# Performance work log

Hardware: AMD Instinct MI355X
Metric: run time of the kernel (lower is better)

The kernel has to match this reference:

```python
import jax, jax.numpy as jnp
import numpy as np


def setup_inputs() -> dict:
    key = jax.random.key(0)
    k_q, k_k, k_v, k_xd, k_yd = jax.random.split(key, 5)
    B, L, H, E, K = 8, 4096, 2048, 512, 64
    return {
        "queries": jax.random.normal(k_q, (B, L, E), dtype=jnp.float32),
        "keys": jax.random.normal(k_k, (B, L, E), dtype=jnp.float32),
        "values": jax.random.normal(k_v, (B, L, E), dtype=jnp.float32),
        "x_date": jax.random.normal(k_xd, (B, L, K), dtype=jnp.float32),
        "y_date": jax.random.normal(k_yd, (B, H, K), dtype=jnp.float32),
    }


def reference(queries, keys, values, x_date, y_date):
    # queries/keys are unused in the original forward's math (only shapes).
    k = x_date.shape[-1]
    scale = 1.0 / float(np.sqrt(k))  # self.scale is None -> 1/sqrt(k)
    # scores: [B, L, H] from date features
    scores = jnp.einsum('blk,bhk->blh', x_date, y_date)
    # softmax over target axis H (dim=-1), numerically stable
    A = jax.nn.softmax(scale * scores, axis=-1)  # [B, L, H]
    # weighted reduction over source axis L -> [B, H, E]
    V = jnp.einsum('ble,blh->bhe', values, A)
    return V
```

## Files before the change

### kernel.cpp

```cpp
#include <hip/hip_runtime.h>
#include <hip/hip_bf16.h>

#define BN 8
#define LN 4096
#define HN 2048
#define EN 512
#define KN 64
#define LT 32
#define NIT 128

typedef __attribute__((ext_vector_type(8))) short bf16x8;
typedef __attribute__((ext_vector_type(4))) float f32x4;
typedef __attribute__((ext_vector_type(4))) unsigned u32x4;

__device__ __forceinline__ short f2b(float x) {
  union { float f; unsigned u; } v; v.f = x;
  unsigned r = v.u + 0x7fffu + ((v.u >> 16) & 1u);
  return (short)(r >> 16);
}

__device__ __forceinline__ bf16x8 cvt8s(const float* __restrict__ p, float s) {
  f32x4 a = *(const f32x4*)(p);
  f32x4 b = *(const f32x4*)(p + 4);
  bf16x8 r;
  r[0] = f2b(a[0] * s); r[1] = f2b(a[1] * s); r[2] = f2b(a[2] * s); r[3] = f2b(a[3] * s);
  r[4] = f2b(b[0] * s); r[5] = f2b(b[1] * s); r[6] = f2b(b[2] * s); r[7] = f2b(b[3] * s);
  return r;
}

__device__ __forceinline__ void gload16(const void* g, void* s) {
  __builtin_amdgcn_global_load_lds(
      (const __attribute__((address_space(1))) unsigned int*)(unsigned long long)g,
      (__attribute__((address_space(3))) unsigned int*)(unsigned int)(unsigned long long)s,
      16, 0, 0);
}

__global__ __launch_bounds__(256) void k_prep(const float* __restrict__ vals,
                                              short* __restrict__ valsT,
                                              const float* __restrict__ xd,
                                              short* __restrict__ xo,
                                              const float* __restrict__ yd,
                                              short* __restrict__ yo,
                                              float* __restrict__ ps) {
  __shared__ unsigned trT[2048];
  const int bx = blockIdx.x;
  const int tid = threadIdx.x;
  const float c0 = 0.125f * 1.4426950408889634f;
  if (bx < 1536) {
    const float* src;
    short* dst;
    float scale;
    int i;
    if (bx < 1024) { i = bx * 256 + tid; src = xd; dst = xo; scale = c0; }
    else           { i = (bx - 1024) * 256 + tid; src = yd; dst = yo; scale = 1.0f; }
    *(bf16x8*)(dst + (size_t)i * 8) = cvt8s(src + (size_t)i * 8, scale);
  } else if (bx < 5632) {
    const int idx = bx - 1536;
    const int b = idx >> 9;
    const int e0 = ((idx >> 6) & 7) * 64;
    const int l0 = (idx & 63) * 64;
    {
      int lr2 = tid >> 3;
      int ec = (tid & 7) * 8;
      const float* r0 = vals + ((size_t)b * LN + l0 + 2 * lr2) * EN + e0 + ec;
      const float* r1 = r0 + EN;
      f32x4 a0 = *(const f32x4*)r0, a1 = *(const f32x4*)(r0 + 4);
      f32x4 cc0 = *(const f32x4*)r1, cc1 = *(const f32x4*)(r1 + 4);
#pragma unroll
      for (int j = 0; j < 8; ++j) {
        float lo = (j < 4) ? a0[j] : a1[j - 4];
        float hi = (j < 4) ? cc0[j] : cc1[j - 4];
        unsigned dw = (unsigned)(unsigned short)f2b(lo) |
                      ((unsigned)(unsigned short)f2b(hi) << 16);
        int e = ec + j;
        int sz = (((e >> 3) ^ e) & 7) << 2;
        trT[e * 32 + (lr2 ^ sz)] = dw;
      }
    }
    __syncthreads();
    {
      int er = tid >> 2, lq = (tid & 3) * 8;
      int sr = ((er >> 3) ^ er) & 7;
      const unsigned* base = trT + er * 32;
      u32x4 u0 = *(const u32x4*)(base + ((((lq >> 2) + 0) ^ sr) << 2));
      u32x4 u1 = *(const u32x4*)(base + ((((lq >> 2) + 1) ^ sr) << 2));
      short* dst = valsT + ((size_t)b * EN + e0 + er) * LN + l0 + 2 * lq;
      *(u32x4*)dst = u0;
      *(u32x4*)(dst + 8) = u1;
    }
  } else {
    const int idx = bx - 5632;
    const int b = (idx >> 5) & 7, hc = idx >> 8;
    const int w = tid >> 6, lane = tid & 63;
    const int row = lane & 15, g = lane >> 4;
    const int lb = (idx & 31) * 128 + w * 32;
    const size_t bL = (size_t)b * LN, bH = (size_t)b * HN;
    bf16x8 xa[2][2];
#pragma unroll
    for (int lt = 0; lt < 2; ++lt) {
      const float* xp = xd + (bL + lb + lt * 16 + row) * KN + g * 8;
      xa[lt][0] = cvt8s(xp, c0);
      xa[lt][1] = cvt8s(xp + 32, c0);
    }
    float s[2][4] = {{0.f, 0.f, 0.f, 0.f}, {0.f, 0.f, 0.f, 0.f}};
    const float* ybase = yd + (bH + hc * 512 + row) * KN + g * 8;
#pragma unroll 2
    for (int it = 0; it < 32; ++it) {
      const float* yp = ybase + (size_t)it * (16 * KN);
      bf16x8 y0 = cvt8s(yp, 1.0f);
      bf16x8 y1 = cvt8s(yp + 32, 1.0f);
#pragma unroll
      for (int lt = 0; lt < 2; ++lt) {
        f32x4 a = {0.f, 0.f, 0.f, 0.f};
        a = __builtin_amdgcn_mfma_f32_16x16x32_bf16(xa[lt][0], y0, a, 0, 0, 0);
        a = __builtin_amdgcn_mfma_f32_16x16x32_bf16(xa[lt][1], y1, a, 0, 0, 0);
#pragma unroll
        for (int r = 0; r < 4; ++r) s[lt][r] += __builtin_amdgcn_exp2f(a[r]);
      }
    }
#pragma unroll
    for (int d = 1; d < 16; d <<= 1)
#pragma unroll
      for (int lt = 0; lt < 2; ++lt)
#pragma unroll
        for (int r = 0; r < 4; ++r) s[lt][r] += __shfl_xor(s[lt][r], d);
    if (row == 0) {
#pragma unroll
      for (int lt = 0; lt < 2; ++lt)
#pragma unroll
        for (int r = 0; r < 4; ++r)
          ps[(size_t)hc * (BN * LN) + bL + lb + lt * 16 + 4 * g + r] = s[lt][r];
    }
  }
}

__global__ void k_comb(const float* __restrict__ ps, float* __restrict__ wv) {
  int idx = blockIdx.x * 256 + threadIdx.x;
  float z = ps[idx] + ps[BN * LN + idx] + ps[2 * BN * LN + idx] + ps[3 * BN * LN + idx];
  wv[idx] = 1.0f / z;
}

__global__ __launch_bounds__(256, 2) void k_main7(
    const short* __restrict__ valsT, const short* __restrict__ xb,
    const short* __restrict__ yb, const float* __restrict__ wv,
    float* __restrict__ out) {
  __shared__ __align__(16) char smem[70016];
  const int tid = threadIdx.x;
  const int w = tid >> 6, lane = tid & 63;
  const int row = lane & 15, g = lane >> 4;

  const int f = blockIdx.x;
  const int b = f & 7;
  const int rest = f >> 3;
  const int hb = (rest & 31) * 64;
  const int eb = (rest >> 5) * 256;
  const size_t bL = (size_t)b * LN, bH = (size_t)b * HN;
  const int wbase = __builtin_amdgcn_readfirstlane(tid & ~63);

  const short* vsrc[4];
#pragma unroll
  for (int j = 0; j < 4; ++j) {
    int i = j * 256 + tid;
    int e = i >> 2, sl = (i & 3) ^ ((e >> 1) & 3);
    vsrc[j] = valsT + (((size_t)b * EN + eb + e) << 12) + 8 * sl;
  }
  const short* xsrc = xb + ((bL + (tid >> 3)) << 6) + 8 * ((tid & 7) ^ ((tid >> 3) & 7));
  const float* ssrc = wv + bL + 4 * tid;

  auto stage = [&](int t) {
    int m3 = t % 3;
    gload16(xsrc + ((size_t)t << 11), smem + 49152 + m3 * 4096 + wbase * 16);
    if (tid < 8)
      gload16(ssrc + t * 32, smem + 69632 + m3 * 128);
#pragma unroll
    for (int j = 0; j < 4; ++j)
      gload16(vsrc[j] + t * 32, smem + m3 * 16384 + j * 4096 + wbase * 16);
  };

  bf16x8 ya0, ya1;
  {
    const short* yp = yb + ((bH + hb + w * 16 + row) << 6) + 8 * g;
    ya0 = *(const bf16x8*)yp;
    ya1 = *(const bf16x8*)(yp + 32);
  }
  int xoffA[2], xoffB[2], poff[2], swoff[2];
#pragma unroll
  for (int lt = 0; lt < 2; ++lt) {
    int lr = lt * 16 + row;
    int sp0 = g ^ (lr & 7);
    xoffA[lt] = (lr << 7) + (sp0 << 4);
    xoffB[lt] = (lr << 7) + ((sp0 ^ 4) << 4);
    int hq1 = w * 16 + row;
    poff[lt] = hq1 * 64 + (((2 * lt + (g >> 1)) ^ ((hq1 >> 1) & 3)) << 4) + (g & 1) * 8;
    swoff[lt] = lt * 16 + 4 * g;
  }

  int paoff[4], vboff[4];
#pragma unroll
  for (int at = 0; at < 4; ++at) {
    int hq = at * 16 + row;
    paoff[at] = hq * 64 + ((g ^ ((hq >> 1) & 3)) << 4);
  }
#pragma unroll
  for (int n = 0; n < 4; ++n) {
    int el = w * 64 + n * 16 + row;
    vboff[n] = el * 64 + ((g ^ ((el >> 1) & 3)) << 4);
  }

  f32x4 acc[4][4];
#pragma unroll
  for (int at = 0; at < 4; ++at)
#pragma unroll
    for (int n = 0; n < 4; ++n) acc[at][n] = (f32x4){0.f, 0.f, 0.f, 0.f};

  auto produce = [&](int t) {
    const char* xbuf = smem + 49152 + (t % 3) * 4096;
    const float* swp = (const float*)(smem + 69632 + (t % 3) * 128);
    char* pdst = smem + 61440 + (t & 1) * 4096;
#pragma unroll
    for (int lt = 0; lt < 2; ++lt) {
      bf16x8 xa0 = *(const bf16x8*)(xbuf + xoffA[lt]);
      bf16x8 xa1 = *(const bf16x8*)(xbuf + xoffB[lt]);
      f32x4 sws = *(const f32x4*)(swp + swoff[lt]);
      f32x4 s4 = {0.f, 0.f, 0.f, 0.f};
      s4 = __builtin_amdgcn_mfma_f32_16x16x32_bf16(xa0, ya0, s4, 0, 0, 0);
      s4 = __builtin_amdgcn_mfma_f32_16x16x32_bf16(xa1, ya1, s4, 0, 0, 0);
      unsigned u0 = (unsigned)(unsigned short)f2b(__builtin_amdgcn_exp2f(s4[0]) * sws[0]) |
                    ((unsigned)(unsigned short)f2b(__builtin_amdgcn_exp2f(s4[1]) * sws[1]) << 16);
      unsigned u1 = (unsigned)(unsigned short)f2b(__builtin_amdgcn_exp2f(s4[2]) * sws[2]) |
                    ((unsigned)(unsigned short)f2b(__builtin_amdgcn_exp2f(s4[3]) * sws[3]) << 16);
      *(unsigned long long*)(pdst + poff[lt]) =
          (unsigned long long)u0 | ((unsigned long long)u1 << 32);
    }
  };

  auto consume = [&](int t) {
    const char* vbuf = smem + (t % 3) * 16384;
    const char* pbuf = smem + 61440 + (t & 1) * 4096;
    bf16x8 pa0 = *(const bf16x8*)(pbuf + paoff[0]);
    bf16x8 pa1 = *(const bf16x8*)(pbuf + paoff[1]);
    bf16x8 pa2 = *(const bf16x8*)(pbuf + paoff[2]);
    bf16x8 pa3 = *(const bf16x8*)(pbuf + paoff[3]);
    bf16x8 vb0 = *(const bf16x8*)(vbuf + vboff[0]);
    bf16x8 vb1 = *(const bf16x8*)(vbuf + vboff[1]);
    bf16x8 vb2 = *(const bf16x8*)(vbuf + vboff[2]);
    bf16x8 vb3 = *(const bf16x8*)(vbuf + vboff[3]);
    __builtin_amdgcn_s_setprio(1);
    acc[0][0] = __builtin_amdgcn_mfma_f32_16x16x32_bf16(pa0, vb0, acc[0][0], 0, 0, 0);
    acc[1][0] = __builtin_amdgcn_mfma_f32_16x16x32_bf16(pa1, vb0, acc[1][0], 0, 0, 0);
    acc[2][0] = __builtin_amdgcn_mfma_f32_16x16x32_bf16(pa2, vb0, acc[2][0], 0, 0, 0);
    acc[3][0] = __builtin_amdgcn_mfma_f32_16x16x32_bf16(pa3, vb0, acc[3][0], 0, 0, 0);
    acc[0][1] = __builtin_amdgcn_mfma_f32_16x16x32_bf16(pa0, vb1, acc[0][1], 0, 0, 0);
    acc[1][1] = __builtin_amdgcn_mfma_f32_16x16x32_bf16(pa1, vb1, acc[1][1], 0, 0, 0);
    acc[2][1] = __builtin_amdgcn_mfma_f32_16x16x32_bf16(pa2, vb1, acc[2][1], 0, 0, 0);
    acc[3][1] = __builtin_amdgcn_mfma_f32_16x16x32_bf16(pa3, vb1, acc[3][1], 0, 0, 0);
    acc[0][2] = __builtin_amdgcn_mfma_f32_16x16x32_bf16(pa0, vb2, acc[0][2], 0, 0, 0);
    acc[1][2] = __builtin_amdgcn_mfma_f32_16x16x32_bf16(pa1, vb2, acc[1][2], 0, 0, 0);
    acc[2][2] = __builtin_amdgcn_mfma_f32_16x16x32_bf16(pa2, vb2, acc[2][2], 0, 0, 0);
    acc[3][2] = __builtin_amdgcn_mfma_f32_16x16x32_bf16(pa3, vb2, acc[3][2], 0, 0, 0);
    acc[0][3] = __builtin_amdgcn_mfma_f32_16x16x32_bf16(pa0, vb3, acc[0][3], 0, 0, 0);
    acc[1][3] = __builtin_amdgcn_mfma_f32_16x16x32_bf16(pa1, vb3, acc[1][3], 0, 0, 0);
    acc[2][3] = __builtin_amdgcn_mfma_f32_16x16x32_bf16(pa2, vb3, acc[2][3], 0, 0, 0);
    acc[3][3] = __builtin_amdgcn_mfma_f32_16x16x32_bf16(pa3, vb3, acc[3][3], 0, 0, 0);
    __builtin_amdgcn_s_setprio(0);
  };

  stage(0);
  stage(1);
  asm volatile("s_waitcnt vmcnt(4)" ::: "memory");
  __builtin_amdgcn_s_barrier();
  asm volatile("" ::: "memory");
  produce(0);
  asm volatile("s_waitcnt lgkmcnt(0)" ::: "memory");
  __builtin_amdgcn_s_barrier();
  asm volatile("" ::: "memory");

  for (int it = 0; it < NIT; ++it) {
    if (it + 2 < NIT) stage(it + 2);
    if (it + 1 < NIT) produce(it + 1);
    consume(it);
    if (it + 1 < NIT) {
      if (it + 2 < NIT)
        asm volatile("s_waitcnt vmcnt(4) lgkmcnt(0)" ::: "memory");
      else
        asm volatile("s_waitcnt vmcnt(0) lgkmcnt(0)" ::: "memory");
      __builtin_amdgcn_s_barrier();
      asm volatile("" ::: "memory");
    }
  }

#pragma unroll
  for (int at = 0; at < 4; ++at)
#pragma unroll
    for (int n = 0; n < 4; ++n)
#pragma unroll
      for (int r = 0; r < 4; ++r) {
        int h = hb + at * 16 + 4 * g + r;
        int e = eb + w * 64 + n * 16 + row;
        out[(bH + h) * (size_t)EN + e] = acc[at][n][r];
      }
}

__global__ __launch_bounds__(256) void k_stats_o(const float* __restrict__ xd,
                                                 const float* __restrict__ yd,
                                                 float* __restrict__ mz) {
  const int b = blockIdx.y;
  const int w = threadIdx.x >> 6;
  const int lane = threadIdx.x & 63;
  const int row = lane & 15, g = lane >> 4;
  const int lb = blockIdx.x * 64 + w * 16;
  const float* xp = xd + ((size_t)b * LN + lb + row) * KN + g * 8;
  bf16x8 a0 = cvt8s(xp, 1.0f), a1 = cvt8s(xp + 32, 1.0f);
  float m[4], s[4];
#pragma unroll
  for (int r = 0; r < 4; ++r) { m[r] = -1e30f; s[r] = 0.f; }
  const float* ybp = yd + ((size_t)b * HN + row) * KN + g * 8;
  for (int h0 = 0; h0 < HN; h0 += 16) {
    bf16x8 b0 = cvt8s(ybp + (size_t)h0 * KN, 1.0f);
    bf16x8 b1 = cvt8s(ybp + (size_t)h0 * KN + 32, 1.0f);
    f32x4 acc = {0.f, 0.f, 0.f, 0.f};
    acc = __builtin_amdgcn_mfma_f32_16x16x32_bf16(a0, b0, acc, 0, 0, 0);
    acc = __builtin_amdgcn_mfma_f32_16x16x32_bf16(a1, b1, acc, 0, 0, 0);
#pragma unroll
    for (int r = 0; r < 4; ++r) {
      float v = acc[r] * 0.125f;
      float mn = fmaxf(m[r], v);
      s[r] = s[r] * __expf(m[r] - mn) + __expf(v - mn);
      m[r] = mn;
    }
  }
#pragma unroll
  for (int d = 1; d < 16; d <<= 1) {
#pragma unroll
    for (int r = 0; r < 4; ++r) {
      float mo = __shfl_xor(m[r], d);
      float so = __shfl_xor(s[r], d);
      float mn = fmaxf(m[r], mo);
      s[r] = s[r] * __expf(m[r] - mn) + so * __expf(mo - mn);
      m[r] = mn;
    }
  }
  if (row == 0) {
#pragma unroll
    for (int r = 0; r < 4; ++r) {
      size_t idx = (size_t)b * LN + lb + 4 * g + r;
      mz[idx] = m[r];
      mz[(size_t)BN * LN + idx] = 1.0f / s[r];
    }
  }
}

__global__ __launch_bounds__(512) void k_main_o(const float* __restrict__ vals,
                                                const float* __restrict__ xd,
                                                const float* __restrict__ yd,
                                                const float* __restrict__ mz,
                                                float* __restrict__ out) {
  __shared__ short vT[256][34];
  __shared__ short pT[128][34];
  __shared__ short xT[32][72];
  __shared__ float smm[32], smz[32];
  const int b = blockIdx.z;
  const int hb = blockIdx.x * 128;
  const int eb = blockIdx.y * 256;
  const int tid = threadIdx.x;
  const int w = tid >> 6, lane = tid & 63;
  const int row = lane & 15, g = lane >> 4;
  const float* yp = yd + ((size_t)b * HN + hb + w * 16 + row) * KN + g * 8;
  bf16x8 ya0 = cvt8s(yp, 1.0f), ya1 = cvt8s(yp + 32, 1.0f);
  f32x4 acc[16];
#pragma unroll
  for (int n = 0; n < 16; ++n) acc[n] = (f32x4){0.f, 0.f, 0.f, 0.f};
  const float* mzb = mz + (size_t)b * LN;
  const float* rzb = mz + (size_t)BN * LN + (size_t)b * LN;
  for (int l0 = 0; l0 < LN; l0 += 32) {
    __syncthreads();
    {
      int xl = tid >> 4, xk = (tid & 15) * 4;
      f32x4 xv = *(const f32x4*)(xd + ((size_t)b * LN + l0 + xl) * KN + xk);
      union { short h[4]; int i[2]; } u;
      u.h[0] = f2b(xv[0]); u.h[1] = f2b(xv[1]); u.h[2] = f2b(xv[2]); u.h[3] = f2b(xv[3]);
      int* dst = (int*)(&xT[xl][xk]);
      dst[0] = u.i[0]; dst[1] = u.i[1];
    }
#pragma unroll
    for (int lp = 0; lp < 4; ++lp) {
      int vl = (tid >> 6) + lp * 8;
      const float* vrow = vals + ((size_t)b * LN + l0 + vl) * EN + eb;
#pragma unroll
      for (int u2 = 0; u2 < 4; ++u2) {
        int e = (tid & 63) + u2 * 64;
        vT[e][vl] = f2b(vrow[e]);
      }
    }
    if (tid < 32) { smm[tid] = mzb[l0 + tid]; smz[tid] = rzb[l0 + tid]; }
    __syncthreads();
#pragma unroll
    for (int t2 = 0; t2 < 2; ++t2) {
      const short* xr = &xT[t2 * 16 + row][0];
      bf16x8 xb0 = *(const bf16x8*)(xr + 8 * g);
      bf16x8 xb1 = *(const bf16x8*)(xr + 32 + 8 * g);
      f32x4 sa = {0.f, 0.f, 0.f, 0.f};
      sa = __builtin_amdgcn_mfma_f32_16x16x32_bf16(ya0, xb0, sa, 0, 0, 0);
      sa = __builtin_amdgcn_mfma_f32_16x16x32_bf16(ya1, xb1, sa, 0, 0, 0);
      int lcol = t2 * 16 + row;
      float mm = smm[lcol], zz = smz[lcol];
#pragma unroll
      for (int r = 0; r < 4; ++r) {
        float p2 = __expf(sa[r] * 0.125f - mm) * zz;
        pT[w * 16 + 4 * g + r][lcol] = f2b(p2);
      }
    }
    __syncthreads();
    bf16x8 pa;
    {
      const int* pi = (const int*)(&pT[w * 16 + row][0] + 8 * g);
      union { int i[4]; bf16x8 f; } u;
      u.i[0] = pi[0]; u.i[1] = pi[1]; u.i[2] = pi[2]; u.i[3] = pi[3];
      pa = u.f;
    }
#pragma unroll
    for (int n = 0; n < 16; ++n) {
      const int* vi = (const int*)(&vT[n * 16 + row][0] + 8 * g);
      union { int i[4]; bf16x8 f; } u;
      u.i[0] = vi[0]; u.i[1] = vi[1]; u.i[2] = vi[2]; u.i[3] = vi[3];
      acc[n] = __builtin_amdgcn_mfma_f32_16x16x32_bf16(pa, u.f, acc[n], 0, 0, 0);
    }
  }
#pragma unroll
  for (int n = 0; n < 16; ++n)
#pragma unroll
    for (int r = 0; r < 4; ++r) {
      int h = hb + w * 16 + 4 * g + r;
      int e = eb + n * 16 + row;
      out[((size_t)b * HN + h) * EN + e] = acc[n][r];
    }
}

extern "C" void kernel_launch(void* const* d_in, const int* in_sizes, int n_in,
                              void* d_out, int out_size, void* d_ws, size_t ws_size,
                              hipStream_t stream) {
  const float* vals = (const float*)d_in[2];
  const float* xd = (const float*)d_in[3];
  const float* yd = (const float*)d_in[4];
  float* out = (float*)d_out;

  if (ws_size >= 40501248ull) {
    char* wsb = (char*)d_ws;
    short* valsT = (short*)wsb;
    short* xbuf  = (short*)(wsb + 33554432);
    short* ybuf  = (short*)(wsb + 37748736);
    float* ps    = (float*)(wsb + 39845888);
    float* wv    = (float*)(wsb + 40370176);

    k_prep<<<dim3(6656), 256, 0, stream>>>(vals, valsT, xd, xbuf, yd, ybuf, ps);
    k_comb<<<dim3(BN * LN / 256), 256, 0, stream>>>(ps, wv);
    k_main7<<<dim3(512), 256, 0, stream>>>(valsT, xbuf, ybuf, wv, out);
  } else {
    float* mz = (float*)d_ws;
    k_stats_o<<<dim3(LN / 64, BN), 256, 0, stream>>>(xd, yd, mz);
    k_main_o<<<dim3(HN / 128, EN / 256, BN), 512, 0, stream>>>(vals, xd, yd, mz, out);
  }
}
```

Measured before the change: 206.1 us.

## Fold softmax weights into bf16 values and switch main loop to 32x32 MFMA in registers

The per-row softmax normalizer is now applied to the values during the bf16 transpose pass, which becomes a separate kernel launched after the normalizer is computed. The main kernel drops its score staging through shared memory: it computes scores with 32x32x16 MFMAs and converts exp2 results to packed bf16. It then uses permlane32 swaps to feed them directly as the A operand of the second MFMA, removing the produce/consume LDS round trip and an extra barrier. This adds a kernel launch and serializes the value transpose behind the normalizer, and rounding the scaled values to bf16 shifts precision slightly.

```diff
diff --git a/kernel.cpp b/kernel.cpp
--- a/kernel.cpp
+++ b/kernel.cpp
@@ -11,6 +11,7 @@
 
 typedef __attribute__((ext_vector_type(8))) short bf16x8;
 typedef __attribute__((ext_vector_type(4))) float f32x4;
+typedef __attribute__((ext_vector_type(16))) float f32x16;
 typedef __attribute__((ext_vector_type(4))) unsigned u32x4;
 
 __device__ __forceinline__ short f2b(float x) {
@@ -35,14 +36,11 @@
       16, 0, 0);
 }
 
-__global__ __launch_bounds__(256) void k_prep(const float* __restrict__ vals,
-                                              short* __restrict__ valsT,
-                                              const float* __restrict__ xd,
-                                              short* __restrict__ xo,
-                                              const float* __restrict__ yd,
-                                              short* __restrict__ yo,
-                                              float* __restrict__ ps) {
-  __shared__ unsigned trT[2048];
+__global__ __launch_bounds__(256) void k_prep1(const float* __restrict__ xd,
+                                               short* __restrict__ xo,
+                                               const float* __restrict__ yd,
+                                               short* __restrict__ yo,
+                                               float* __restrict__ ps) {
   const int bx = blockIdx.x;
   const int tid = threadIdx.x;
   const float c0 = 0.125f * 1.4426950408889634f;
@@ -54,42 +52,8 @@
     if (bx < 1024) { i = bx * 256 + tid; src = xd; dst = xo; scale = c0; }
     else           { i = (bx - 1024) * 256 + tid; src = yd; dst = yo; scale = 1.0f; }
     *(bf16x8*)(dst + (size_t)i * 8) = cvt8s(src + (size_t)i * 8, scale);
-  } else if (bx < 5632) {
+  } else {
     const int idx = bx - 1536;
-    const int b = idx >> 9;
-    const int e0 = ((idx >> 6) & 7) * 64;
-    const int l0 = (idx & 63) * 64;
-    {
-      int lr2 = tid >> 3;
-      int ec = (tid & 7) * 8;
-      const float* r0 = vals + ((size_t)b * LN + l0 + 2 * lr2) * EN + e0 + ec;
-      const float* r1 = r0 + EN;
-      f32x4 a0 = *(const f32x4*)r0, a1 = *(const f32x4*)(r0 + 4);
-      f32x4 cc0 = *(const f32x4*)r1, cc1 = *(const f32x4*)(r1 + 4);
-#pragma unroll
-      for (int j = 0; j < 8; ++j) {
-        float lo = (j < 4) ? a0[j] : a1[j - 4];
-        float hi = (j < 4) ? cc0[j] : cc1[j - 4];
-        unsigned dw = (unsigned)(unsigned short)f2b(lo) |
-                      ((unsigned)(unsigned short)f2b(hi) << 16);
-        int e = ec + j;
-        int sz = (((e >> 3) ^ e) & 7) << 2;
-        trT[e * 32 + (lr2 ^ sz)] = dw;
-      }
-    }
-    __syncthreads();
-    {
-      int er = tid >> 2, lq = (tid & 3) * 8;
-      int sr = ((er >> 3) ^ er) & 7;
-      const unsigned* base = trT + er * 32;
-      u32x4 u0 = *(const u32x4*)(base + ((((lq >> 2) + 0) ^ sr) << 2));
-      u32x4 u1 = *(const u32x4*)(base + ((((lq >> 2) + 1) ^ sr) << 2));
-      short* dst = valsT + ((size_t)b * EN + e0 + er) * LN + l0 + 2 * lq;
-      *(u32x4*)dst = u0;
-      *(u32x4*)(dst + 8) = u1;
-    }
-  } else {
-    const int idx = bx - 5632;
     const int b = (idx >> 5) & 7, hc = idx >> 8;
     const int w = tid >> 6, lane = tid & 63;
     const int row = lane & 15, g = lane >> 4;
@@ -140,14 +104,55 @@
   wv[idx] = 1.0f / z;
 }
 
-__global__ __launch_bounds__(256, 2) void k_main7(
+__global__ __launch_bounds__(256) void k_prep2(const float* __restrict__ vals,
+                                               const float* __restrict__ wv,
+                                               short* __restrict__ valsT) {
+  __shared__ unsigned trT[2048];
+  const int idx = blockIdx.x;
+  const int tid = threadIdx.x;
+  const int b = idx >> 9;
+  const int e0 = ((idx >> 6) & 7) * 64;
+  const int l0 = (idx & 63) * 64;
+  {
+    int lr2 = tid >> 3;
+    int ec = (tid & 7) * 8;
+    const float* r0 = vals + ((size_t)b * LN + l0 + 2 * lr2) * EN + e0 + ec;
+    const float* r1 = r0 + EN;
+    float w0 = wv[(size_t)b * LN + l0 + 2 * lr2];
+    float w1 = wv[(size_t)b * LN + l0 + 2 * lr2 + 1];
+    f32x4 a0 = *(const f32x4*)r0, a1 = *(const f32x4*)(r0 + 4);
+    f32x4 cc0 = *(const f32x4*)r1, cc1 = *(const f32x4*)(r1 + 4);
+#pragma unroll
+    for (int j = 0; j < 8; ++j) {
+      float lo = ((j < 4) ? a0[j] : a1[j - 4]) * w0;
+      float hi = ((j < 4) ? cc0[j] : cc1[j - 4]) * w1;
+      unsigned dw = (unsigned)(unsigned short)f2b(lo) |
+                    ((unsigned)(unsigned short)f2b(hi) << 16);
+      int e = ec + j;
+      int sz = (((e >> 3) ^ e) & 7) << 2;
+      trT[e * 32 + (lr2 ^ sz)] = dw;
+    }
+  }
+  __syncthreads();
+  {
+    int er = tid >> 2, lq = (tid & 3) * 8;
+    int sr = ((er >> 3) ^ er) & 7;
+    const unsigned* base = trT + er * 32;
+    u32x4 u0 = *(const u32x4*)(base + ((((lq >> 2) + 0) ^ sr) << 2));
+    u32x4 u1 = *(const u32x4*)(base + ((((lq >> 2) + 1) ^ sr) << 2));
+    short* dst = valsT + ((size_t)b * EN + e0 + er) * LN + l0 + 2 * lq;
+    *(u32x4*)dst = u0;
+    *(u32x4*)(dst + 8) = u1;
+  }
+}
+
+__global__ __launch_bounds__(256, 2) void k_main8(
     const short* __restrict__ valsT, const short* __restrict__ xb,
-    const short* __restrict__ yb, const float* __restrict__ wv,
-    float* __restrict__ out) {
-  __shared__ __align__(16) char smem[70016];
+    const short* __restrict__ yb, float* __restrict__ out) {
+  __shared__ __align__(16) char smem[61440];
   const int tid = threadIdx.x;
   const int w = tid >> 6, lane = tid & 63;
-  const int row = lane & 15, g = lane >> 4;
+  const int l5 = lane & 31, hi = lane >> 5;
 
   const int f = blockIdx.x;
   const int b = f & 7;
@@ -155,133 +160,103 @@
   const int hb = (rest & 31) * 64;
   const int eb = (rest >> 5) * 256;
   const size_t bL = (size_t)b * LN, bH = (size_t)b * HN;
-  const int wbase = __builtin_amdgcn_readfirstlane(tid & ~63);
+  const int hh = w >> 1, eq = w & 1;
 
   const short* vsrc[4];
 #pragma unroll
   for (int j = 0; j < 4; ++j) {
     int i = j * 256 + tid;
-    int e = i >> 2, sl = (i & 3) ^ ((e >> 1) & 3);
+    int e = i >> 2, c = i & 3, sl = c ^ (e & 3);
     vsrc[j] = valsT + (((size_t)b * EN + eb + e) << 12) + 8 * sl;
   }
   const short* xsrc = xb + ((bL + (tid >> 3)) << 6) + 8 * ((tid & 7) ^ ((tid >> 3) & 7));
-  const float* ssrc = wv + bL + 4 * tid;
 
   auto stage = [&](int t) {
     int m3 = t % 3;
-    gload16(xsrc + ((size_t)t << 11), smem + 49152 + m3 * 4096 + wbase * 16);
-    if (tid < 8)
-      gload16(ssrc + t * 32, smem + 69632 + m3 * 128);
+    gload16(xsrc + ((size_t)t << 11), smem + 49152 + m3 * 4096 + tid * 16);
 #pragma unroll
     for (int j = 0; j < 4; ++j)
-      gload16(vsrc[j] + t * 32, smem + m3 * 16384 + j * 4096 + wbase * 16);
+      gload16(vsrc[j] + t * 32, smem + m3 * 16384 + (j * 256 + tid) * 16);
   };
 
-  bf16x8 ya0, ya1;
+  bf16x8 ya[4];
   {
-    const short* yp = yb + ((bH + hb + w * 16 + row) << 6) + 8 * g;
-    ya0 = *(const bf16x8*)yp;
-    ya1 = *(const bf16x8*)(yp + 32);
-  }
-  int xoffA[2], xoffB[2], poff[2], swoff[2];
-#pragma unroll
-  for (int lt = 0; lt < 2; ++lt) {
-    int lr = lt * 16 + row;
-    int sp0 = g ^ (lr & 7);
-    xoffA[lt] = (lr << 7) + (sp0 << 4);
-    xoffB[lt] = (lr << 7) + ((sp0 ^ 4) << 4);
-    int hq1 = w * 16 + row;
-    poff[lt] = hq1 * 64 + (((2 * lt + (g >> 1)) ^ ((hq1 >> 1) & 3)) << 4) + (g & 1) * 8;
-    swoff[lt] = lt * 16 + 4 * g;
-  }
-
-  int paoff[4], vboff[4];
-#pragma unroll
-  for (int at = 0; at < 4; ++at) {
-    int hq = at * 16 + row;
-    paoff[at] = hq * 64 + ((g ^ ((hq >> 1) & 3)) << 4);
-  }
-#pragma unroll
-  for (int n = 0; n < 4; ++n) {
-    int el = w * 64 + n * 16 + row;
-    vboff[n] = el * 64 + ((g ^ ((el >> 1) & 3)) << 4);
-  }
-
-  f32x4 acc[4][4];
-#pragma unroll
-  for (int at = 0; at < 4; ++at)
-#pragma unroll
-    for (int n = 0; n < 4; ++n) acc[at][n] = (f32x4){0.f, 0.f, 0.f, 0.f};
-
-  auto produce = [&](int t) {
-    const char* xbuf = smem + 49152 + (t % 3) * 4096;
-    const float* swp = (const float*)(smem + 69632 + (t % 3) * 128);
-    char* pdst = smem + 61440 + (t & 1) * 4096;
-#pragma unroll
-    for (int lt = 0; lt < 2; ++lt) {
-      bf16x8 xa0 = *(const bf16x8*)(xbuf + xoffA[lt]);
-      bf16x8 xa1 = *(const bf16x8*)(xbuf + xoffB[lt]);
-      f32x4 sws = *(const f32x4*)(swp + swoff[lt]);
-      f32x4 s4 = {0.f, 0.f, 0.f, 0.f};
-      s4 = __builtin_amdgcn_mfma_f32_16x16x32_bf16(xa0, ya0, s4, 0, 0, 0);
-      s4 = __builtin_amdgcn_mfma_f32_16x16x32_bf16(xa1, ya1, s4, 0, 0, 0);
-      unsigned u0 = (unsigned)(unsigned short)f2b(__builtin_amdgcn_exp2f(s4[0]) * sws[0]) |
-                    ((unsigned)(unsigned short)f2b(__builtin_amdgcn_exp2f(s4[1]) * sws[1]) << 16);
-      unsigned u1 = (unsigned)(unsigned short)f2b(__builtin_amdgcn_exp2f(s4[2]) * sws[2]) |
-                    ((unsigned)(unsigned short)f2b(__builtin_amdgcn_exp2f(s4[3]) * sws[3]) << 16);
-      *(unsigned long long*)(pdst + poff[lt]) =
-          (unsigned long long)u0 | ((unsigned long long)u1 << 32);
-    }
-  };
-
-  auto consume = [&](int t) {
-    const char* vbuf = smem + (t % 3) * 16384;
-    const char* pbuf = smem + 61440 + (t & 1) * 4096;
-    bf16x8 pa0 = *(const bf16x8*)(pbuf + paoff[0]);
-    bf16x8 pa1 = *(const bf16x8*)(pbuf + paoff[1]);
-    bf16x8 pa2 = *(const bf16x8*)(pbuf + paoff[2]);
-    bf16x8 pa3 = *(const bf16x8*)(pbuf + paoff[3]);
-    bf16x8 vb0 = *(const bf16x8*)(vbuf + vboff[0]);
-    bf16x8 vb1 = *(const bf16x8*)(vbuf + vboff[1]);
-    bf16x8 vb2 = *(const bf16x8*)(vbuf + vboff[2]);
-    bf16x8 vb3 = *(const bf16x8*)(vbuf + vboff[3]);
-    __builtin_amdgcn_s_setprio(1);
-    acc[0][0] = __builtin_amdgcn_mfma_f32_16x16x32_bf16(pa0, vb0, acc[0][0], 0, 0, 0);
-    acc[1][0] = __builtin_amdgcn_mfma_f32_16x16x32_bf16(pa1, vb0, acc[1][0], 0, 0, 0);
-    acc[2][0] = __builtin_amdgcn_mfma_f32_16x16x32_bf16(pa2, vb0, acc[2][0], 0, 0, 0);
-    acc[3][0] = __builtin_amdgcn_mfma_f32_16x16x32_bf16(pa3, vb0, acc[3][0], 0, 0, 0);
-    acc[0][1] = __builtin_amdgcn_mfma_f32_16x16x32_bf16(pa0, vb1, acc[0][1], 0, 0, 0);
-    acc[1][1] = __builtin_amdgcn_mfma_f32_16x16x32_bf16(pa1, vb1, acc[1][1], 0, 0, 0);
-    acc[2][1] = __builtin_amdgcn_mfma_f32_16x16x32_bf16(pa2, vb1, acc[2][1], 0, 0, 0);
-    acc[3][1] = __builtin_amdgcn_mfma_f32_16x16x32_bf16(pa3, vb1, acc[3][1], 0, 0, 0);
-    acc[0][2] = __builtin_amdgcn_mfma_f32_16x16x32_bf16(pa0, vb2, acc[0][2], 0, 0, 0);
-    acc[1][2] = __builtin_amdgcn_mfma_f32_16x16x32_bf16(pa1, vb2, acc[1][2], 0, 0, 0);
-    acc[2][2] = __builtin_amdgcn_mfma_f32_16x16x32_bf16(pa2, vb2, acc[2][2], 0, 0, 0);
-    acc[3][2] = __builtin_amdgcn_mfma_f32_16x16x32_bf16(pa3, vb2, acc[3][2], 0, 0, 0);
-    acc[0][3] = __builtin_amdgcn_mfma_f32_16x16x32_bf16(pa0, vb3, acc[0][3], 0, 0, 0);
-    acc[1][3] = __builtin_amdgcn_mfma_f32_16x16x32_bf16(pa1, vb3, acc[1][3], 0, 0, 0);
-    acc[2][3] = __builtin_amdgcn_mfma_f32_16x16x32_bf16(pa2, vb3, acc[2][3], 0, 0, 0);
-    acc[3][3] = __builtin_amdgcn_mfma_f32_16x16x32_bf16(pa3, vb3, acc[3][3], 0, 0, 0);
-    __builtin_amdgcn_s_setprio(0);
-  };
+    const short* yp = yb + ((bH + hb + hh * 32 + l5) << 6) + hi * 8;
+#pragma unroll
+    for (int kf = 0; kf < 4; ++kf) ya[kf] = *(const bf16x8*)(yp + kf * 16);
+  }
+  int xoff[4];
+#pragma unroll
+  for (int kf = 0; kf < 4; ++kf)
+    xoff[kf] = l5 * 128 + (((2 * kf + hi) ^ (l5 & 7)) << 4);
+  int voff[4][2];
+#pragma unroll
+  for (int et = 0; et < 4; ++et) {
+    int e = eq * 128 + et * 32 + l5;
+#pragma unroll
+    for (int kh = 0; kh < 2; ++kh)
+      voff[et][kh] = e * 64 + (((2 * kh + hi) ^ (e & 3)) << 4);
+  }
+
+  f32x16 acc[4];
+#pragma unroll
+  for (int et = 0; et < 4; ++et)
+#pragma unroll
+    for (int q = 0; q < 16; ++q) acc[et][q] = 0.f;
 
   stage(0);
   stage(1);
-  asm volatile("s_waitcnt vmcnt(4)" ::: "memory");
+  asm volatile("s_waitcnt vmcnt(5)" ::: "memory");
   __builtin_amdgcn_s_barrier();
   asm volatile("" ::: "memory");
-  produce(0);
-  asm volatile("s_waitcnt lgkmcnt(0)" ::: "memory");
-  __builtin_amdgcn_s_barrier();
-  asm volatile("" ::: "memory");
 
   for (int it = 0; it < NIT; ++it) {
+    const char* vbuf = smem + (it % 3) * 16384;
+    const char* xbuf = smem + 49152 + (it % 3) * 4096;
     if (it + 2 < NIT) stage(it + 2);
-    if (it + 1 < NIT) produce(it + 1);
-    consume(it);
-    if (it + 1 < NIT) {
-      if (it + 2 < NIT)
-        asm volatile("s_waitcnt vmcnt(4) lgkmcnt(0)" ::: "memory");
+
+    bf16x8 vb[4][2];
+#pragma unroll
+    for (int et = 0; et < 4; ++et) {
+      vb[et][0] = *(const bf16x8*)(vbuf + voff[et][0]);
+      vb[et][1] = *(const bf16x8*)(vbuf + voff[et][1]);
+    }
+
+    f32x16 d;
+#pragma unroll
+    for (int q = 0; q < 16; ++q) d[q] = 0.f;
+#pragma unroll
+    for (int kf = 0; kf < 4; ++kf) {
+      bf16x8 xa = *(const bf16x8*)(xbuf + xoff[kf]);
+      d = __builtin_amdgcn_mfma_f32_32x32x16_bf16(xa, ya[kf], d, 0, 0, 0);
+    }
+
+    int dw[8];
+#pragma unroll
+    for (int q = 0; q < 8; ++q) {
+      float plo = __builtin_amdgcn_exp2f(d[2 * q]);
+      float phi = __builtin_amdgcn_exp2f(d[2 * q + 1]);
+      asm("v_cvt_pk_bf16_f32 %0, %1, %2" : "=v"(dw[q]) : "v"(plo), "v"(phi));
+    }
+    asm volatile("v_permlane32_swap_b32 %0, %1" : "+v"(dw[0]), "+v"(dw[2]));
+    asm volatile("v_permlane32_swap_b32 %0, %1" : "+v"(dw[1]), "+v"(dw[3]));
+    asm volatile("v_permlane32_swap_b32 %0, %1" : "+v"(dw[4]), "+v"(dw[6]));
+    asm volatile("v_permlane32_swap_b32 %0, %1" : "+v"(dw[5]), "+v"(dw[7]));
+    union { int i[4]; bf16x8 v; } pa0, pa1;
+    pa0.i[0] = dw[0]; pa0.i[1] = dw[1]; pa0.i[2] = dw[2]; pa0.i[3] = dw[3];
+    pa1.i[0] = dw[4]; pa1.i[1] = dw[5]; pa1.i[2] = dw[6]; pa1.i[3] = dw[7];
+
+    __builtin_amdgcn_s_setprio(1);
+#pragma unroll
+    for (int et = 0; et < 4; ++et) {
+      acc[et] = __builtin_amdgcn_mfma_f32_32x32x16_bf16(pa0.v, vb[et][0], acc[et], 0, 0, 0);
+      acc[et] = __builtin_amdgcn_mfma_f32_32x32x16_bf16(pa1.v, vb[et][1], acc[et], 0, 0, 0);
+    }
+    __builtin_amdgcn_s_setprio(0);
+
+    if (it < NIT - 1) {
+      if (it < NIT - 2)
+        asm volatile("s_waitcnt vmcnt(5) lgkmcnt(0)" ::: "memory");
       else
         asm volatile("s_waitcnt vmcnt(0) lgkmcnt(0)" ::: "memory");
       __builtin_amdgcn_s_barrier();
@@ -290,15 +265,13 @@
   }
 
 #pragma unroll
-  for (int at = 0; at < 4; ++at)
-#pragma unroll
-    for (int n = 0; n < 4; ++n)
-#pragma unroll
-      for (int r = 0; r < 4; ++r) {
-        int h = hb + at * 16 + 4 * g + r;
-        int e = eb + w * 64 + n * 16 + row;
-        out[(bH + h) * (size_t)EN + e] = acc[at][n][r];
-      }
+  for (int et = 0; et < 4; ++et)
+#pragma unroll
+    for (int r = 0; r < 16; ++r) {
+      int h = hb + hh * 32 + (r & 3) + 8 * (r >> 2) + 4 * hi;
+      int e = eb + eq * 128 + et * 32 + l5;
+      out[(bH + h) * (size_t)EN + e] = acc[et][r];
+    }
 }
 
 __global__ __launch_bounds__(256) void k_stats_o(const float* __restrict__ xd,
@@ -452,9 +425,10 @@
     float* ps    = (float*)(wsb + 39845888);
     float* wv    = (float*)(wsb + 40370176);
 
-    k_prep<<<dim3(6656), 256, 0, stream>>>(vals, valsT, xd, xbuf, yd, ybuf, ps);
+    k_prep1<<<dim3(2560), 256, 0, stream>>>(xd, xbuf, yd, ybuf, ps);
     k_comb<<<dim3(BN * LN / 256), 256, 0, stream>>>(ps, wv);
-    k_main7<<<dim3(512), 256, 0, stream>>>(valsT, xbuf, ybuf, wv, out);
+    k_prep2<<<dim3(4096), 256, 0, stream>>>(vals, wv, valsT);
+    k_main8<<<dim3(512), 256, 0, stream>>>(valsT, xbuf, ybuf, out);
   } else {
     float* mz = (float*)d_ws;
     k_stats_o<<<dim3(LN / 64, BN), 256, 0, stream>>>(xd, yd, mz);
```

Measured after the change: 224.4 us. 1.09x slower.
